# Kernel tuning notes

Measured on AMD Instinct MI355X. Metric: run time of the kernel, lower is better.

## Reference

```python
import jax, jax.numpy as jnp
import numpy as np

B, S, D, H, NS = 4, 2048, 1024, 16, 300
DK = D // H                      # 64
NSP = (NS + H - 1) // H * H      # 304 (padded skills)
DG = NSP // H                    # 19
NEG_FILL = -1e9                  # fp32 path in the torch module


def setup_inputs() -> dict:
    key = jax.random.key(0)
    ks = jax.random.split(key, 12)
    sc = 0.02
    return {
        "context_sequence": jax.random.normal(ks[0], (B, S, D), jnp.float32),
        "value_sequence": jax.random.normal(ks[1], (B, S, NS), jnp.float32),
        "mask": jnp.triu(jnp.ones((S, S), jnp.bool_), k=1),  # causal: True = masked
        # weights stored as [in, out] (math-equivalent to torch's x @ W.T + b)
        "Wq": jax.random.normal(ks[2], (D, D), jnp.float32) * sc,
        "bq": jnp.zeros((D,), jnp.float32),
        "Wk": jax.random.normal(ks[3], (D, D), jnp.float32) * sc,
        "bk": jnp.zeros((D,), jnp.float32),
        "Wv": jax.random.normal(ks[4], (NS, NS), jnp.float32) * sc,
        "bv": jnp.zeros((NS,), jnp.float32),
        "Wg": jax.random.normal(ks[5], (NS, D), jnp.float32) * sc,  # gain_to_context
        "bg": jnp.zeros((D,), jnp.float32),
        "Wo": jax.random.normal(ks[6], (D, D), jnp.float32) * sc,   # output_proj
        "bo": jnp.zeros((D,), jnp.float32),
    }


def reference(context_sequence, value_sequence, mask,
              Wq, bq, Wk, bk, Wv, bv, Wg, bg, Wo, bo):
    b = context_sequence.shape[0]
    orig_dtype = context_sequence.dtype

    # Q, K: [b, H, S, DK]
    Q = (context_sequence @ Wq + bq).reshape(b, -1, H, DK).transpose(0, 2, 1, 3)
    K = (context_sequence @ Wk + bk).reshape(b, -1, H, DK).transpose(0, 2, 1, 3)

    # intrinsic-gain V: project in skill space, zero-pad to NSP, split heads -> [b, H, S, DG]
    V_proj = value_sequence @ Wv + bv
    V_proj = jnp.pad(V_proj, ((0, 0), (0, 0), (0, NSP - NS)))
    V = V_proj.reshape(b, -1, H, DG).transpose(0, 2, 1, 3)

    # fp32 score upcast, scale by sqrt(d_k), mask, cast back, softmax
    scores = jnp.einsum('bhqd,bhkd->bhqk',
                        Q.astype(jnp.float32), K.astype(jnp.float32)) / np.sqrt(DK)
    scores = jnp.where(mask, NEG_FILL, scores).astype(orig_dtype)
    attn = jax.nn.softmax(scores, axis=-1)

    # [b, H, S, DG] -> [b, S, NSP] -> slice to NS
    head_gains = jnp.einsum('bhqk,bhkd->bhqd', attn, V)
    agg = head_gains.transpose(0, 2, 1, 3).reshape(b, -1, NSP)[..., :NS]

    output = agg @ Wg + bg            # gain_to_context
    return output @ Wo + bo           # output_proj (dropout is identity in eval)
```

## Files before the change

### kernel.cpp

```cpp
#include <hip/hip_runtime.h>
#include <hip/hip_bf16.h>

#define MROWS 8192
#define DMODEL 1024
#define SLEN 2048
#define NHEADS 16
#define DKH 64
#define DGH 19
#define NSKILL 300
#define KGPAD 320
#define AGG_LD 320
#define QK_LD 2048
#define VK 320
#define VTN 384

typedef __attribute__((ext_vector_type(8))) short short8;
typedef __attribute__((ext_vector_type(4))) float floatx4;

__device__ __forceinline__ float bf2f(unsigned short u) {
  union { unsigned int i; float f; } cv;
  cv.i = ((unsigned int)u) << 16;
  return cv.f;
}
__device__ __forceinline__ unsigned short f2bf(float f) {
  __hip_bfloat16 h = __float2bfloat16(f);
  unsigned short u;
  __builtin_memcpy(&u, &h, 2);
  return u;
}

__device__ __forceinline__ float exp2hw(float x) {
#if __has_builtin(__builtin_amdgcn_exp2f)
  return __builtin_amdgcn_exp2f(x);
#else
  return __expf(x * 0.6931471805599453f);
#endif
}
__device__ __forceinline__ unsigned int cvt_pk_bf16(float lo, float hi) {
  unsigned int r;
  asm("v_cvt_pk_bf16_f32 %0, %1, %2" : "=v"(r) : "v"(lo), "v"(hi));
  return r;
}

__device__ __forceinline__ void ld8(const float* p, float* v) {
  float4 a = *(const float4*)p;
  float4 b = *((const float4*)p + 1);
  v[0]=a.x; v[1]=a.y; v[2]=a.z; v[3]=a.w;
  v[4]=b.x; v[5]=b.y; v[6]=b.z; v[7]=b.w;
}
__device__ __forceinline__ void st1(float* p, float v) { *p = v; }
__device__ __forceinline__ void st1(__hip_bfloat16* p, float v) {
  unsigned short raw = f2bf(v); __builtin_memcpy(p, &raw, 2);
}
__device__ __forceinline__ void st8(__hip_bfloat16* p, const float* v) {
  ushort4 a, b;
  a.x=f2bf(v[0]); a.y=f2bf(v[1]); a.z=f2bf(v[2]); a.w=f2bf(v[3]);
  b.x=f2bf(v[4]); b.y=f2bf(v[5]); b.z=f2bf(v[6]); b.w=f2bf(v[7]);
  *(ushort4*)p = a;
  *((ushort4*)p + 1) = b;
}

__device__ __forceinline__ void gl_lds16(const void* g, void* l) {
  __builtin_amdgcn_global_load_lds(
      (const __attribute__((address_space(1))) unsigned int*)g,
      (__attribute__((address_space(3))) unsigned int*)l, 16, 0, 0);
}

__global__ __launch_bounds__(256)
void prep_mega_kernel(const float* __restrict__ X,
                      const float* __restrict__ Vin,
                      const float* __restrict__ Wg,
                      const float* __restrict__ bq, const float* __restrict__ bk,
                      const float* __restrict__ bv,
                      const float* __restrict__ Wq, const float* __restrict__ Wk,
                      const float* __restrict__ Wo, const float* __restrict__ Wv,
                      __hip_bfloat16* __restrict__ Xb,
                      __hip_bfloat16* __restrict__ Vb16,
                      __hip_bfloat16* __restrict__ Wgb,
                      float* __restrict__ biasqk, float* __restrict__ biasv,
                      float* __restrict__ z384,
                      __hip_bfloat16* __restrict__ Wtqk,
                      __hip_bfloat16* __restrict__ WoT,
                      __hip_bfloat16* __restrict__ Wvt)
{
  const int bid = blockIdx.x;
  const int t = threadIdx.x;
  if (bid < 8192) {
    int i = (bid * 256 + t) * 4;
    float4 v = *(const float4*)(X + i);
    ushort4 s;
    s.x = f2bf(v.x); s.y = f2bf(v.y); s.z = f2bf(v.z); s.w = f2bf(v.w);
    *(ushort4*)((__hip_bfloat16*)Xb + i) = s;
    return;
  }
  if (bid < 9472) {
    int idx = (bid - 8192) * 256 + t;
    int row = idx / 40;
    int c8  = (idx - row * 40) * 8;
    const float* ip = Vin + (size_t)row * NSKILL + c8;
    float v[8];
    if (c8 + 8 <= NSKILL) {
      ld8(ip, v);
    } else {
      #pragma unroll
      for (int u = 0; u < 8; u++)
        v[u] = (c8 + u < NSKILL) ? ip[u] : 0.f;
    }
    st8(Vb16 + (size_t)row * VK + c8, v);
    return;
  }
  if (bid < 9856) {
    int i4 = ((bid - 9472) * 256 + t) * 4;
    int r = i4 >> 10;
    ushort4 s = {0, 0, 0, 0};
    if (r < NSKILL) {
      float4 v = *(const float4*)(Wg + i4);
      s.x = f2bf(v.x); s.y = f2bf(v.y); s.z = f2bf(v.z); s.w = f2bf(v.w);
    }
    *(ushort4*)((__hip_bfloat16*)Wgb + i4) = s;
    return;
  }
  if (bid == 9856) {
    for (int i = t; i < 1024; i += 256) { biasqk[i] = bq[i]; biasqk[1024 + i] = bk[i]; }
    for (int i = t; i < 384; i += 256) {
      biasv[i] = (i < NSKILL) ? bv[i] : 0.f;
      z384[i] = 0.f;
    }
    return;
  }
  const float* W; __hip_bfloat16* Wt; int K, Nld, Ntrue, Kpad, kx, ny;
  if (bid < 10881)      { int l = bid - 9857;  W=Wq; Wt=Wtqk;            K=1024; Nld=1024; Ntrue=1024; Kpad=1024; kx=l&31; ny=l>>5; }
  else if (bid < 11905) { int l = bid - 10881; W=Wk; Wt=Wtqk+1024*1024;  K=1024; Nld=1024; Ntrue=1024; Kpad=1024; kx=l&31; ny=l>>5; }
  else if (bid < 12929) { int l = bid - 11905; W=Wo; Wt=WoT;             K=1024; Nld=1024; Ntrue=1024; Kpad=1024; kx=l&31; ny=l>>5; }
  else                  { int l = bid - 12929; W=Wv; Wt=Wvt;             K=NSKILL; Nld=NSKILL; Ntrue=NSKILL; Kpad=VK; kx=l%10; ny=l/10; }
  __shared__ float tb[32][33];
  const int k0 = kx * 32;
  const int n0 = ny * 32;
  const int tx = t & 31, ty = t >> 5;
  #pragma unroll
  for (int i = 0; i < 4; i++) {
    int k = k0 + ty + i*8;
    int nn = n0 + tx;
    tb[ty + i*8][tx] = (k < K && nn < Ntrue) ? W[(size_t)k * Nld + nn] : 0.f;
  }
  __syncthreads();
  #pragma unroll
  for (int i = 0; i < 4; i++) {
    int nn = n0 + ty + i*8;
    int kk = k0 + tx;
    st1(Wt + (size_t)nn * Kpad + kk, tb[tx][ty + i*8]);
  }
}

__device__ __forceinline__ void gemm_core(const short* __restrict__ Ag,
                                          const short* __restrict__ Bg,
                                          int lda, int ldb, int K,
                                          int m0, int n0,
                                          short* Al, short* Bl,
                                          int tid, floatx4 (&acc)[4][4])
{
  const int lane = tid & 63;
  const int wave = tid >> 6;
  const int wy = wave >> 1, wx = wave & 1;
  const int n = lane & 15;
  const int quad = lane >> 4;

  for (int k0 = 0; k0 < K; k0 += 64) {
    #pragma unroll
    for (int it = 0; it < 4; it++) {
      int ci = it*256 + tid;
      int r = ci >> 3, c = ci & 7;
      int cs = c ^ (r & 7);
      gl_lds16(Ag + (size_t)(m0 + r) * lda + k0 + cs*8, &Al[ci*8]);
    }
    #pragma unroll
    for (int it = 0; it < 4; it++) {
      int ci = it*256 + tid;
      int r = ci >> 3, c = ci & 7;
      int cs = c ^ (r & 7);
      gl_lds16(Bg + (size_t)(n0 + r) * ldb + k0 + cs*8, &Bl[ci*8]);
    }
    __syncthreads();

    #pragma unroll
    for (int s = 0; s < 2; s++) {
      short8 af[4], bfr[4];
      const int c = s*4 + quad;
      #pragma unroll
      for (int i = 0; i < 4; i++) {
        int r = wy*64 + i*16 + n;
        af[i] = *(const short8*)&Al[(r*8 + (c ^ (r & 7)))*8];
      }
      #pragma unroll
      for (int j = 0; j < 4; j++) {
        int r = wx*64 + j*16 + n;
        bfr[j] = *(const short8*)&Bl[(r*8 + (c ^ (r & 7)))*8];
      }
      #pragma unroll
      for (int i = 0; i < 4; i++)
        #pragma unroll
        for (int j = 0; j < 4; j++)
          acc[i][j] = __builtin_amdgcn_mfma_f32_16x16x32_bf16(af[i], bfr[j], acc[i][j], 0, 0, 0);
    }
    __syncthreads();
  }
}

__global__ __launch_bounds__(256)
void gemm_qk_vt_kernel(const __hip_bfloat16* __restrict__ Xb,
                       const __hip_bfloat16* __restrict__ Wtqk,
                       const float* __restrict__ biasqk,
                       __hip_bfloat16* __restrict__ QKbuf,
                       const __hip_bfloat16* __restrict__ Vb16,
                       const __hip_bfloat16* __restrict__ Wvt,
                       const float* __restrict__ biasv,
                       __hip_bfloat16* __restrict__ VT)
{
  __shared__ __align__(16) short Al[128*64];
  __shared__ __align__(16) short Bl[128*64];
  const int tid = threadIdx.x;
  const int lane = tid & 63;
  const int wave = tid >> 6;
  const int wy = wave >> 1, wx = wave & 1;
  const int n = lane & 15;
  const int quad = lane >> 4;

  floatx4 acc[4][4];
  #pragma unroll
  for (int i = 0; i < 4; i++)
    #pragma unroll
    for (int j = 0; j < 4; j++) acc[i][j] = (floatx4){0.f,0.f,0.f,0.f};

  if (blockIdx.x < 1024) {
    const int bx = blockIdx.x & 15, by = blockIdx.x >> 4;
    const int m0 = by * 128, n0 = bx * 128;
    gemm_core((const short*)Xb, (const short*)Wtqk, DMODEL, DMODEL, DMODEL,
              m0, n0, Al, Bl, tid, acc);
    float bj[4];
    #pragma unroll
    for (int j = 0; j < 4; j++) bj[j] = biasqk[n0 + wx*64 + j*16 + n];
    #pragma unroll
    for (int i = 0; i < 4; i++) {
      #pragma unroll
      for (int r = 0; r < 4; r++) {
        int row = m0 + wy*64 + i*16 + quad*4 + r;
        __hip_bfloat16* cp = QKbuf + (size_t)row * QK_LD;
        #pragma unroll
        for (int j = 0; j < 4; j++) {
          int col = n0 + wx*64 + j*16 + n;
          st1(cp + col, acc[i][j][r] + bj[j]);
        }
      }
    }
  } else {
    const int l = blockIdx.x - 1024;
    const int bx = l % 3, by = l / 3;
    const int m0 = by * 128, n0 = bx * 128;
    gemm_core((const short*)Vb16, (const short*)Wvt, VK, VK, VK,
              m0, n0, Al, Bl, tid, acc);
    float bj[4];
    #pragma unroll
    for (int j = 0; j < 4; j++) bj[j] = biasv[n0 + wx*64 + j*16 + n];
    #pragma unroll
    for (int i = 0; i < 4; i++) {
      int row0 = m0 + wy*64 + i*16 + quad*4;
      int bb = row0 >> 11, rin = row0 & 2047;
      #pragma unroll
      for (int j = 0; j < 4; j++) {
        int col = n0 + wx*64 + j*16 + n;
        ushort4 pk;
        pk.x = f2bf(acc[i][j][0] + bj[j]);
        pk.y = f2bf(acc[i][j][1] + bj[j]);
        pk.z = f2bf(acc[i][j][2] + bj[j]);
        pk.w = f2bf(acc[i][j][3] + bj[j]);
        *(ushort4*)(VT + ((size_t)bb * VTN + col) * SLEN + rin) = pk;
      }
    }
  }
}

__global__ __launch_bounds__(256)
void wgo_bgo_kernel(const __hip_bfloat16* __restrict__ WoT,
                    const __hip_bfloat16* __restrict__ Wgb,
                    const float* __restrict__ z384,
                    __hip_bfloat16* __restrict__ WgoT,
                    const float* __restrict__ bg, const float* __restrict__ Wo,
                    const float* __restrict__ bo, float* __restrict__ bgo)
{
  __shared__ __align__(16) short Al[128*64];
  __shared__ __align__(16) short Bl[128*64];
  const int tid = threadIdx.x;
  if (blockIdx.x < 24) {
    const int lane = tid & 63;
    const int wave = tid >> 6;
    const int wy = wave >> 1, wx = wave & 1;
    const int n = lane & 15;
    const int quad = lane >> 4;
    const int bx = blockIdx.x % 3, by = blockIdx.x / 3;
    const int m0 = by * 128, n0 = bx * 128;
    floatx4 acc[4][4];
    #pragma unroll
    for (int i = 0; i < 4; i++)
      #pragma unroll
      for (int j = 0; j < 4; j++) acc[i][j] = (floatx4){0.f,0.f,0.f,0.f};
    gemm_core((const short*)WoT, (const short*)Wgb, DMODEL, DMODEL, DMODEL,
              m0, n0, Al, Bl, tid, acc);
    float bj[4];
    #pragma unroll
    for (int j = 0; j < 4; j++) bj[j] = z384[n0 + wx*64 + j*16 + n];
    #pragma unroll
    for (int i = 0; i < 4; i++) {
      #pragma unroll
      for (int r = 0; r < 4; r++) {
        int row = m0 + wy*64 + i*16 + quad*4 + r;
        __hip_bfloat16* cp = WgoT + (size_t)row * 384;
        #pragma unroll
        for (int j = 0; j < 4; j++) {
          int col = n0 + wx*64 + j*16 + n;
          st1(cp + col, acc[i][j][r] + bj[j]);
        }
      }
    }
  } else {
    __shared__ float red[256];
    const int c   = tid & 15;
    const int jg  = tid >> 4;
    const int col = (blockIdx.x - 24) * 16 + c;
    float acc = 0.f;
    const int j0 = jg * 64;
    #pragma unroll 8
    for (int j = j0; j < j0 + 64; j++)
      acc = fmaf(bg[j], Wo[(size_t)j * DMODEL + col], acc);
    red[tid] = acc;
    __syncthreads();
    if (jg == 0) {
      float s = 0.f;
      #pragma unroll
      for (int g = 0; g < 16; g++) s += red[g*16 + c];
      bgo[col] = s + bo[col];
    }
  }
}

__global__ __launch_bounds__(256)
void gemm_final_kernel(const __hip_bfloat16* __restrict__ A,
                       const __hip_bfloat16* __restrict__ Bt,
                       const float* __restrict__ bias,
                       float* __restrict__ C)
{
  __shared__ __align__(16) short Al[128*64];
  __shared__ __align__(16) short Bl[128*64];
  const int tid = threadIdx.x;
  const int lane = tid & 63;
  const int wave = tid >> 6;
  const int wy = wave >> 1, wx = wave & 1;
  const int n = lane & 15;
  const int quad = lane >> 4;
  const int m0 = blockIdx.y * 128;
  const int n0 = blockIdx.x * 128;
  floatx4 acc[4][4];
  #pragma unroll
  for (int i = 0; i < 4; i++)
    #pragma unroll
    for (int j = 0; j < 4; j++) acc[i][j] = (floatx4){0.f,0.f,0.f,0.f};
  gemm_core((const short*)A, (const short*)Bt, KGPAD, 384, KGPAD,
            m0, n0, Al, Bl, tid, acc);
  float bj[4];
  #pragma unroll
  for (int j = 0; j < 4; j++) bj[j] = bias[n0 + wx*64 + j*16 + n];
  #pragma unroll
  for (int i = 0; i < 4; i++) {
    #pragma unroll
    for (int r = 0; r < 4; r++) {
      int row = m0 + wy*64 + i*16 + quad*4 + r;
      float* cp = C + (size_t)row * DMODEL;
      #pragma unroll
      for (int j = 0; j < 4; j++) {
        int col = n0 + wx*64 + j*16 + n;
        cp[col] = acc[i][j][r] + bj[j];
      }
    }
  }
}

#define ATT_BM 128
#define ATT_BK 64
#define ATT_GRID 1024

__global__ __launch_bounds__(256)
void attn_mfma_kernel(const __hip_bfloat16* __restrict__ Qb,
                      const __hip_bfloat16* __restrict__ Kb,
                      const __hip_bfloat16* __restrict__ VTg,
                      __hip_bfloat16* __restrict__ Agg)
{
  __shared__ __align__(16) short Kf[2][64*64];
  __shared__ __align__(16) short Vf[2][32*64];
  __shared__ __align__(16) unsigned int Pl[4][2][2][4][16][4];

  const int tid  = threadIdx.x;
  const int lane = tid & 63;
  const int wave = tid >> 6;
  const int n    = lane & 15;
  const int quad = lane >> 4;

  const int raw = blockIdx.x;
  const int grp = raw >> 6;
  const int qt  = (grp < 8) ? (15 - grp) : (grp - 8);
  const int bh  = raw & 63;
  const int h   = bh & 15;
  const int b   = bh >> 4;
  const int qbase = qt * ATT_BM;
  const size_t bS = (size_t)b * SLEN;

  const float QSCALE = 0.18033688f;
  short8 qf[2][2];
  #pragma unroll
  for (int rf = 0; rf < 2; rf++)
    #pragma unroll
    for (int ks = 0; ks < 2; ks++) {
      const __hip_bfloat16* qp = Qb + (bS + qbase + wave*32 + rf*16 + n) * QK_LD
                                    + h*DKH + ks*32 + quad*8;
      short8 v = *(const short8*)qp;
      #pragma unroll
      for (int e = 0; e < 8; e++) {
        float f = bf2f((unsigned short)v[e]) * QSCALE;
        v[e] = (short)f2bf(f);
      }
      qf[rf][ks] = v;
    }

  const short* kp;
  {
    int f = tid;
    int nn = f & 15, q = (f >> 4) & 3, c = (f >> 6) & 3;
    kp = (const short*)Kb + (bS + c*16 + nn) * QK_LD + h*DKH + q*8;
  }
  const short* vp;
  {
    int g = tid;
    int vn = g & 15, vq = (g >> 4) & 3, sv = (g >> 6) & 1, cv = g >> 7;
    vp = (const short*)VTg + ((size_t)b * VTN + h*DGH + cv*16 + vn) * SLEN
         + sv*32 + vq*8;
  }

  floatx4 of[2][2];
  float mrow[2], lrow[2];
  #pragma unroll
  for (int rf = 0; rf < 2; rf++) {
    #pragma unroll
    for (int cv = 0; cv < 2; cv++) of[rf][cv] = (floatx4){0.f,0.f,0.f,0.f};
    mrow[rf] = -1e30f; lrow[rf] = 0.f;
  }

  const int ntiles = (qbase + ATT_BM) / ATT_BK;
  const int wrow_max = qbase + wave*32 + 31;

  auto stage = [&](int buf) {
    gl_lds16(kp,      &Kf[buf][tid*8]);
    gl_lds16(kp + 32, &Kf[buf][(tid + 256)*8]);
    gl_lds16(vp,      &Vf[buf][tid*8]);
    kp += 64 * QK_LD;
    vp += 64;
  };

  auto compute_tile = [&](int buf, int kbase) {
    if (kbase > wrow_max) return;
    short8 kfr[4][2];
    #pragma unroll
    for (int cf = 0; cf < 4; cf++)
      #pragma unroll
      for (int s = 0; s < 2; s++)
        kfr[cf][s] = *(const short8*)&Kf[buf][((s*4 + cf)*64 + lane)*8];

    floatx4 sf[2][4];
    __builtin_amdgcn_s_setprio(1);
    #pragma unroll
    for (int rf = 0; rf < 2; rf++)
      #pragma unroll
      for (int cf = 0; cf < 4; cf++) {
        floatx4 a2 = (floatx4){0.f,0.f,0.f,0.f};
        a2 = __builtin_amdgcn_mfma_f32_16x16x32_bf16(kfr[cf][0], qf[rf][0], a2, 0, 0, 0);
        a2 = __builtin_amdgcn_mfma_f32_16x16x32_bf16(kfr[cf][1], qf[rf][1], a2, 0, 0, 0);
        sf[rf][cf] = a2;
      }
    __builtin_amdgcn_s_setprio(0);

    #pragma unroll
    for (int rf = 0; rf < 2; rf++) {
      const int qrow = qbase + wave*32 + rf*16 + n;
      if (kbase + 63 > qbase + wave*32 + rf*16) {
        #pragma unroll
        for (int cf = 0; cf < 4; cf++)
          #pragma unroll
          for (int r = 0; r < 4; r++) {
            int key = kbase + cf*16 + quad*4 + r;
            if (key > qrow) sf[rf][cf][r] = -INFINITY;
          }
      }
      float m0 = fmaxf(sf[rf][0][0], sf[rf][0][1]);
      #pragma unroll
      for (int i = 2; i < 16; i += 2)
        m0 = fmaxf(fmaxf(m0, sf[rf][i>>2][i&3]), sf[rf][(i+1)>>2][(i+1)&3]);
      m0 = fmaxf(m0, __shfl_xor(m0, 16));
      m0 = fmaxf(m0, __shfl_xor(m0, 32));
      float mnew = fmaxf(mrow[rf], m0);
      float alpha = exp2hw(mrow[rf] - mnew);
      mrow[rf] = mnew;
      float rs = 0.f;
      #pragma unroll
      for (int cf = 0; cf < 4; cf++)
        #pragma unroll
        for (int r = 0; r < 4; r++) {
          float p = exp2hw(sf[rf][cf][r] - mnew);
          sf[rf][cf][r] = p;
          rs += p;
        }
      rs += __shfl_xor(rs, 16);
      rs += __shfl_xor(rs, 32);
      lrow[rf] = lrow[rf] * alpha + rs;
      #pragma unroll
      for (int cv = 0; cv < 2; cv++)
        #pragma unroll
        for (int r = 0; r < 4; r++) of[rf][cv][r] *= alpha;

      #pragma unroll
      for (int cf = 0; cf < 4; cf++) {
        unsigned int w0 = cvt_pk_bf16(sf[rf][cf][0], sf[rf][cf][1]);
        unsigned int w1 = cvt_pk_bf16(sf[rf][cf][2], sf[rf][cf][3]);
        int s   = cf >> 1;
        int qt2 = 2*(cf & 1) + (quad >> 1);
        int jp  = 2*(quad & 1);
        *(uint2*)&Pl[wave][rf][s][qt2][n][jp] = make_uint2(w0, w1);
      }
    }

    short8 vfr[2][2];
    #pragma unroll
    for (int cv = 0; cv < 2; cv++)
      #pragma unroll
      for (int s = 0; s < 2; s++)
        vfr[cv][s] = *(const short8*)&Vf[buf][((cv*2 + s)*64 + lane)*8];

    __builtin_amdgcn_s_setprio(1);
    #pragma unroll
    for (int rf = 0; rf < 2; rf++) {
      short8 p0 = *(const short8*)&Pl[wave][rf][0][quad][n][0];
      short8 p1 = *(const short8*)&Pl[wave][rf][1][quad][n][0];
      #pragma unroll
      for (int cv = 0; cv < 2; cv++) {
        floatx4 a2 = of[rf][cv];
        a2 = __builtin_amdgcn_mfma_f32_16x16x32_bf16(vfr[cv][0], p0, a2, 0, 0, 0);
        a2 = __builtin_amdgcn_mfma_f32_16x16x32_bf16(vfr[cv][1], p1, a2, 0, 0, 0);
        of[rf][cv] = a2;
      }
    }
    __builtin_amdgcn_s_setprio(0);
  };

  stage(0);
  for (int kt = 0; kt < ntiles; kt += 2) {
    stage(1);
    asm volatile("s_waitcnt vmcnt(3)" ::: "memory");
    __builtin_amdgcn_s_barrier();
    __builtin_amdgcn_sched_barrier(0);
    compute_tile(0, kt * ATT_BK);
    __builtin_amdgcn_sched_barrier(0);
    __builtin_amdgcn_s_barrier();

    if (kt + 2 < ntiles) {
      stage(0);
      asm volatile("s_waitcnt vmcnt(3)" ::: "memory");
    } else {
      asm volatile("s_waitcnt vmcnt(0)" ::: "memory");
    }
    __builtin_amdgcn_s_barrier();
    __builtin_amdgcn_sched_barrier(0);
    compute_tile(1, (kt + 1) * ATT_BK);
    __builtin_amdgcn_sched_barrier(0);
    __builtin_amdgcn_s_barrier();
  }

  #pragma unroll
  for (int rf = 0; rf < 2; rf++) {
    float inv = 1.f / lrow[rf];
    int row = qbase + wave*32 + rf*16 + n;
    __hip_bfloat16* op = Agg + (bS + row)*AGG_LD + h*DGH;
    #pragma unroll
    for (int cv = 0; cv < 2; cv++)
      #pragma unroll
      for (int r = 0; r < 4; r++) {
        int dim = cv*16 + quad*4 + r;
        if (dim < DGH) st1(op + dim, of[rf][cv][r] * inv);
      }
  }

  if (h == 15) {
    int row = qbase + (tid >> 1);
    int c0 = 304 + (tid & 1) * 8;
    float z[8] = {0.f,0.f,0.f,0.f,0.f,0.f,0.f,0.f};
    st8(Agg + (bS + row)*AGG_LD + c0, z);
  }
}

extern "C" void kernel_launch(void* const* d_in, const int* in_sizes, int n_in,
                              void* d_out, int out_size, void* d_ws, size_t ws_size,
                              hipStream_t stream) {
  const float* X   = (const float*)d_in[0];
  const float* Vin = (const float*)d_in[1];
  const float* Wq  = (const float*)d_in[3];
  const float* bq  = (const float*)d_in[4];
  const float* Wk  = (const float*)d_in[5];
  const float* bk  = (const float*)d_in[6];
  const float* Wv  = (const float*)d_in[7];
  const float* bv  = (const float*)d_in[8];
  const float* Wg  = (const float*)d_in[9];
  const float* bg  = (const float*)d_in[10];
  const float* Wo  = (const float*)d_in[11];
  const float* bo  = (const float*)d_in[12];
  float* out = (float*)d_out;

  char* ws = (char*)d_ws;
  __hip_bfloat16* Xb    = (__hip_bfloat16*)(ws);
  __hip_bfloat16* AggB  = (__hip_bfloat16*)(ws);
  __hip_bfloat16* WgoT  = (__hip_bfloat16*)(ws + 12582912);
  float*          bgoW  = (float*)         (ws + 13369344);
  __hip_bfloat16* QKbuf = (__hip_bfloat16*)(ws + 16777216);
  __hip_bfloat16* WoT   = (__hip_bfloat16*)(ws + 50331648);

  char* ob = (char*)d_out;
  __hip_bfloat16* Wtqk   = (__hip_bfloat16*)(ob);
  float*          biasqk = (float*)(ob + 4194304);
  __hip_bfloat16* Vb16   = (__hip_bfloat16*)(ob + 4202496);
  float*          biasv  = (float*)(ob + 9445376);
  float*          z384   = (float*)(ob + 9446912);
  __hip_bfloat16* Wgb    = (__hip_bfloat16*)(ob + 9448448);
  __hip_bfloat16* Wvt    = (__hip_bfloat16*)(ob + 10234880);
  __hip_bfloat16* VT     = (__hip_bfloat16*)(ob + 12582912);

  dim3 blk(256);
  prep_mega_kernel<<<dim3(13049), blk, 0, stream>>>(
      X, Vin, Wg, bq, bk, bv, Wq, Wk, Wo, Wv,
      Xb, Vb16, Wgb, biasqk, biasv, z384, Wtqk, WoT, Wvt);

  gemm_qk_vt_kernel<<<dim3(1216), blk, 0, stream>>>(
      Xb, Wtqk, biasqk, QKbuf, Vb16, Wvt, biasv, VT);

  wgo_bgo_kernel<<<dim3(88), blk, 0, stream>>>(
      WoT, Wgb, z384, WgoT, bg, Wo, bo, bgoW);

  attn_mfma_kernel<<<dim3(ATT_GRID), dim3(256), 0, stream>>>(
      QKbuf, QKbuf + 1024, VT, AggB);

  gemm_final_kernel<<<dim3(8, 64), blk, 0, stream>>>(AggB, WgoT, bgoW, out);
}
```

Measured before the change: 276.3 us.

## Split long causal attention rows across two blocks with partial-softmax combine

Query tiles 8-15, which have the longest causal key ranges, are now split into two key halves handled by separate blocks. Each half writes its unnormalized output plus running max and sum to scratch space in the output buffer, and a new combine kernel merges them flash-decoding style. Short tiles are paired with split halves so every block does a similar amount of work, which shortens the tail of the attention kernel. The cost is an extra kernel launch and the fp32 partial results written to and read back from global memory.

```diff
diff --git a/kernel.cpp b/kernel.cpp
--- a/kernel.cpp
+++ b/kernel.cpp
@@ -385,17 +385,19 @@
 
 #define ATT_BM 128
 #define ATT_BK 64
-#define ATT_GRID 1024
+#define ATT_GRID (24*64)
 
 __global__ __launch_bounds__(256)
 void attn_mfma_kernel(const __hip_bfloat16* __restrict__ Qb,
                       const __hip_bfloat16* __restrict__ Kb,
                       const __hip_bfloat16* __restrict__ VTg,
-                      __hip_bfloat16* __restrict__ Agg)
+                      __hip_bfloat16* __restrict__ Agg,
+                      float* __restrict__ Pm, float* __restrict__ Pl,
+                      float* __restrict__ Po)
 {
   __shared__ __align__(16) short Kf[2][64*64];
   __shared__ __align__(16) short Vf[2][32*64];
-  __shared__ __align__(16) unsigned int Pl[4][2][2][4][16][4];
+  __shared__ __align__(16) unsigned int Plds[4][2][2][4][16][4];
 
   const int tid  = threadIdx.x;
   const int lane = tid & 63;
@@ -403,12 +405,19 @@
   const int n    = lane & 15;
   const int quad = lane >> 4;
 
-  const int raw = blockIdx.x;
-  const int grp = raw >> 6;
-  const int qt  = (grp < 8) ? (15 - grp) : (grp - 8);
-  const int bh  = raw & 63;
+  const int cid = blockIdx.x >> 6;
+  const int bh  = blockIdx.x & 63;
   const int h   = bh & 15;
   const int b   = bh >> 4;
+  int qt, kt0, nt, mode;
+  if (cid == 0)      { qt = 7;       kt0 = 0;  nt = 16; mode = 0; }
+  else if (cid <= 8) { qt = cid + 7; kt0 = 0;  nt = 16; mode = 1; }
+  else if (cid == 9) { qt = 15;      kt0 = 16; nt = 16; mode = 2; }
+  else {
+    int e = (cid - 10) >> 1;
+    if (((cid - 10) & 1) == 0) { qt = 6 - e;  kt0 = 0;  nt = 14 - 2*e; mode = 0; }
+    else                       { qt = 14 - e; kt0 = 16; nt = 14 - 2*e; mode = 2; }
+  }
   const int qbase = qt * ATT_BM;
   const size_t bS = (size_t)b * SLEN;
 
@@ -433,14 +442,14 @@
   {
     int f = tid;
     int nn = f & 15, q = (f >> 4) & 3, c = (f >> 6) & 3;
-    kp = (const short*)Kb + (bS + c*16 + nn) * QK_LD + h*DKH + q*8;
+    kp = (const short*)Kb + (bS + kt0*64 + c*16 + nn) * QK_LD + h*DKH + q*8;
   }
   const short* vp;
   {
     int g = tid;
     int vn = g & 15, vq = (g >> 4) & 3, sv = (g >> 6) & 1, cv = g >> 7;
     vp = (const short*)VTg + ((size_t)b * VTN + h*DGH + cv*16 + vn) * SLEN
-         + sv*32 + vq*8;
+         + kt0*64 + sv*32 + vq*8;
   }
 
   floatx4 of[2][2];
@@ -452,7 +461,6 @@
     mrow[rf] = -1e30f; lrow[rf] = 0.f;
   }
 
-  const int ntiles = (qbase + ATT_BM) / ATT_BK;
   const int wrow_max = qbase + wave*32 + 31;
 
   auto stage = [&](int buf) {
@@ -530,7 +538,7 @@
         int s   = cf >> 1;
         int qt2 = 2*(cf & 1) + (quad >> 1);
         int jp  = 2*(quad & 1);
-        *(uint2*)&Pl[wave][rf][s][qt2][n][jp] = make_uint2(w0, w1);
+        *(uint2*)&Plds[wave][rf][s][qt2][n][jp] = make_uint2(w0, w1);
       }
     }
 
@@ -544,8 +552,8 @@
     __builtin_amdgcn_s_setprio(1);
     #pragma unroll
     for (int rf = 0; rf < 2; rf++) {
-      short8 p0 = *(const short8*)&Pl[wave][rf][0][quad][n][0];
-      short8 p1 = *(const short8*)&Pl[wave][rf][1][quad][n][0];
+      short8 p0 = *(const short8*)&Plds[wave][rf][0][quad][n][0];
+      short8 p1 = *(const short8*)&Plds[wave][rf][1][quad][n][0];
       #pragma unroll
       for (int cv = 0; cv < 2; cv++) {
         floatx4 a2 = of[rf][cv];
@@ -558,16 +566,16 @@
   };
 
   stage(0);
-  for (int kt = 0; kt < ntiles; kt += 2) {
+  for (int kt = 0; kt < nt; kt += 2) {
     stage(1);
     asm volatile("s_waitcnt vmcnt(3)" ::: "memory");
     __builtin_amdgcn_s_barrier();
     __builtin_amdgcn_sched_barrier(0);
-    compute_tile(0, kt * ATT_BK);
+    compute_tile(0, (kt0 + kt) * ATT_BK);
     __builtin_amdgcn_sched_barrier(0);
     __builtin_amdgcn_s_barrier();
 
-    if (kt + 2 < ntiles) {
+    if (kt + 2 < nt) {
       stage(0);
       asm volatile("s_waitcnt vmcnt(3)" ::: "memory");
     } else {
@@ -575,30 +583,78 @@
     }
     __builtin_amdgcn_s_barrier();
     __builtin_amdgcn_sched_barrier(0);
-    compute_tile(1, (kt + 1) * ATT_BK);
+    compute_tile(1, (kt0 + kt + 1) * ATT_BK);
     __builtin_amdgcn_sched_barrier(0);
     __builtin_amdgcn_s_barrier();
   }
 
-  #pragma unroll
-  for (int rf = 0; rf < 2; rf++) {
-    float inv = 1.f / lrow[rf];
-    int row = qbase + wave*32 + rf*16 + n;
-    __hip_bfloat16* op = Agg + (bS + row)*AGG_LD + h*DGH;
-    #pragma unroll
-    for (int cv = 0; cv < 2; cv++)
-      #pragma unroll
-      for (int r = 0; r < 4; r++) {
-        int dim = cv*16 + quad*4 + r;
-        if (dim < DGH) st1(op + dim, of[rf][cv][r] * inv);
-      }
-  }
-
+  if (mode == 0) {
+    #pragma unroll
+    for (int rf = 0; rf < 2; rf++) {
+      float inv = 1.f / lrow[rf];
+      int row = qbase + wave*32 + rf*16 + n;
+      __hip_bfloat16* op = Agg + (bS + row)*AGG_LD + h*DGH;
+      #pragma unroll
+      for (int cv = 0; cv < 2; cv++)
+        #pragma unroll
+        for (int r = 0; r < 4; r++) {
+          int dim = cv*16 + quad*4 + r;
+          if (dim < DGH) st1(op + dim, of[rf][cv][r] * inv);
+        }
+    }
+    if (h == 15) {
+      int row = qbase + (tid >> 1);
+      int c0 = 304 + (tid & 1) * 8;
+      float z[8] = {0.f,0.f,0.f,0.f,0.f,0.f,0.f,0.f};
+      st8(Agg + (bS + row)*AGG_LD + c0, z);
+    }
+  } else {
+    const int p = (qt - 8) * 64 + bh;
+    const int sl = mode - 1;
+    #pragma unroll
+    for (int rf = 0; rf < 2; rf++) {
+      int rowl = wave*32 + rf*16 + n;
+      size_t ri = (size_t)(sl*512 + p)*128 + rowl;
+      float* po = Po + ri*20;
+      #pragma unroll
+      for (int cv = 0; cv < 2; cv++)
+        #pragma unroll
+        for (int r = 0; r < 4; r++) {
+          int dim = cv*16 + quad*4 + r;
+          if (dim < DGH) po[dim] = of[rf][cv][r];
+        }
+      if (quad == 0) { Pm[ri] = mrow[rf]; Pl[ri] = lrow[rf]; }
+    }
+  }
+}
+
+__global__ __launch_bounds__(256)
+void attn_combine_kernel(const float* __restrict__ Pm, const float* __restrict__ Pl,
+                         const float* __restrict__ Po,
+                         __hip_bfloat16* __restrict__ Agg)
+{
+  int idx = blockIdx.x * 256 + threadIdx.x;
+  int p = idx >> 7, rowl = idx & 127;
+  int qt = 8 + (p >> 6), bh = p & 63, h = bh & 15, b = bh >> 4;
+  size_t riA = (size_t)p*128 + rowl;
+  size_t riB = (size_t)(512 + p)*128 + rowl;
+  float mA = Pm[riA], mB = Pm[riB];
+  float lA = Pl[riA], lB = Pl[riB];
+  float m = fmaxf(mA, mB);
+  float wA = exp2hw(mA - m), wB = exp2hw(mB - m);
+  float inv = 1.f / (wA*lA + wB*lB);
+  wA *= inv; wB *= inv;
+  const float* oA = Po + riA*20;
+  const float* oB = Po + riB*20;
+  size_t row = (size_t)b*SLEN + qt*128 + rowl;
+  __hip_bfloat16* op = Agg + row*AGG_LD + h*DGH;
+  #pragma unroll
+  for (int d = 0; d < DGH; d++)
+    st1(op + d, wA*oA[d] + wB*oB[d]);
   if (h == 15) {
-    int row = qbase + (tid >> 1);
-    int c0 = 304 + (tid & 1) * 8;
-    float z[8] = {0.f,0.f,0.f,0.f,0.f,0.f,0.f,0.f};
-    st8(Agg + (bS + row)*AGG_LD + c0, z);
+    uint4 z = {0,0,0,0};
+    *(uint4*)(Agg + row*AGG_LD + 304) = z;
+    *(uint4*)(Agg + row*AGG_LD + 312) = z;
   }
 }
 
@@ -635,6 +691,9 @@
   float*          z384   = (float*)(ob + 9446912);
   __hip_bfloat16* Wgb    = (__hip_bfloat16*)(ob + 9448448);
   __hip_bfloat16* Wvt    = (__hip_bfloat16*)(ob + 10234880);
+  float*          Pm     = (float*)(ob);
+  float*          Pl     = (float*)(ob + 524288);
+  float*          Po     = (float*)(ob + 1048576);
   __hip_bfloat16* VT     = (__hip_bfloat16*)(ob + 12582912);
 
   dim3 blk(256);
@@ -649,7 +708,9 @@
       WoT, Wgb, z384, WgoT, bg, Wo, bo, bgoW);
 
   attn_mfma_kernel<<<dim3(ATT_GRID), dim3(256), 0, stream>>>(
-      QKbuf, QKbuf + 1024, VT, AggB);
+      QKbuf, QKbuf + 1024, VT, AggB, Pm, Pl, Po);
+
+  attn_combine_kernel<<<dim3(256), blk, 0, stream>>>(Pm, Pl, Po, AggB);
 
   gemm_final_kernel<<<dim3(8, 64), blk, 0, stream>>>(AggB, WgoT, bgoW, out);
 }
```

New measurement: 279.9 us. Within noise of the previous version (+1.3%).
